# Optimization experiments

Hardware: AMD Instinct MI355X
Metric: run time of the kernel (lower is better)

## Reference

```python
import jax, jax.numpy as jnp
import numpy as np

B, N, D, D_OUT = 4, 512, 48, 48

def setup_inputs() -> dict:
    key = jax.random.key(0)
    ks = jax.random.split(key, 7)
    s1 = 1.0 / np.sqrt(2 * D)
    s2 = 1.0 / np.sqrt(2 * D)
    s3 = 1.0 / np.sqrt(D)
    return {
        "x": jax.random.normal(ks[0], (B, N, D), dtype=jnp.float32),
        "W1": jax.random.uniform(ks[1], (2 * D, 2 * D), jnp.float32, -s1, s1),
        "b1": jax.random.uniform(ks[2], (2 * D,), jnp.float32, -s1, s1),
        "W2": jax.random.uniform(ks[3], (2 * D, D), jnp.float32, -s2, s2),
        "b2": jax.random.uniform(ks[4], (D,), jnp.float32, -s2, s2),
        "W3": jax.random.uniform(ks[5], (D, D_OUT), jnp.float32, -s3, s3),
        "b3": jax.random.uniform(ks[6], (D_OUT,), jnp.float32, -s3, s3),
    }

def reference(x, W1, b1, W2, b2, W3, b3):
    # x: [B, N, D]
    Bn, Nn, Dn = x.shape
    xi = jnp.broadcast_to(x[:, :, None, :], (Bn, Nn, Nn, Dn))  # row i
    xj = jnp.broadcast_to(x[:, None, :, :], (Bn, Nn, Nn, Dn))  # col j
    pair = jnp.concatenate([xi, xj], axis=-1)  # [B,N,N,2D]
    h = jax.nn.gelu(pair @ W1 + b1, approximate=False)
    h = jax.nn.gelu(h @ W2 + b2, approximate=False)
    pair_out = h @ W3 + b3  # [B,N,N,d_out]
    mask = jnp.triu(jnp.ones((Nn, Nn), dtype=bool), 1)  # j > i masked
    pair_out = jnp.where(mask[None, :, :, None], 0.0, pair_out)
    w = jnp.linalg.norm(pair_out, axis=-1)  # [B,N,N]
    w = jnp.where(mask[None, :, :], -1e9, w)
    w = jax.nn.softmax(w, axis=-1)
    return jnp.einsum('bnj,bnjd->bnd', w, pair_out)
```

## Files before the change

### kernel.cpp

```cpp
#include <hip/hip_runtime.h>
#include <hip/hip_bf16.h>


constexpr int BATCH = 4;
constexpr int SEQ   = 512;
constexpr int DIM   = 48;
constexpr int DIM2  = 96;
constexpr int CH    = 64;

constexpr int AW  = 104;
constexpr int HW  = 72;

typedef short short8v __attribute__((ext_vector_type(8)));
typedef float float4v __attribute__((ext_vector_type(4)));
typedef unsigned int uint2v __attribute__((ext_vector_type(2)));
typedef unsigned int uint4v __attribute__((ext_vector_type(4)));

#define MFMA16(a, b, c) __builtin_amdgcn_mfma_f32_16x16x32_bf16(a, b, c, 0, 0, 0)

__device__ __forceinline__ float gelu_tanh(float x) {
    float u = x * x;
    float q = fmaf(0.10294537f, u, 2.3022077f);
    float e = __builtin_amdgcn_exp2f(x * q);
    float r = __builtin_amdgcn_rcpf(e + 1.0f);
    return fmaf(-x, r, x);
}
__device__ __forceinline__ short f2bf1(float v) {
    return (short)((__float_as_uint(v) + 0x8000u) >> 16);
}
__device__ __forceinline__ unsigned pack_bf16x2(float a, float b) {
    unsigned ua = __float_as_uint(a) + 0x8000u;
    unsigned ub = __float_as_uint(b) + 0x8000u;
    return __builtin_amdgcn_perm(ub, ua, 0x07060302u);
}
constexpr float LOG2E = 1.4426950408889634f;

__global__ __launch_bounds__(192) void uv_kernel(
    const float* __restrict__ x, const float* __restrict__ W1,
    const float* __restrict__ b1, float* __restrict__ U, float* __restrict__ V)
{
    __shared__ float sxT[DIM * 4];
    const int t = threadIdx.x;
    const int row0 = blockIdx.x * 4;
    if (t < DIM * 4) {
        int r = t / DIM, m = t - r * DIM;
        sxT[m * 4 + r] = x[(row0 + r) * DIM + m];
    }
    __syncthreads();
    const bool isU = (t < DIM2);
    const int  k   = isU ? t : (t - DIM2);
    const float* Wcol = W1 + (isU ? 0 : DIM * DIM2) + k;
    float binit = isU ? b1[k] : 0.0f;
    float a0 = binit, a1 = binit, a2 = binit, a3 = binit;
    #pragma unroll 8
    for (int m = 0; m < DIM; ++m) {
        float wv = Wcol[m * DIM2];
        const float4 xa = *(const float4*)&sxT[m * 4];
        a0 = fmaf(wv, xa.x, a0); a1 = fmaf(wv, xa.y, a1);
        a2 = fmaf(wv, xa.z, a2); a3 = fmaf(wv, xa.w, a3);
    }
    float* dst = isU ? U : V;
    dst[(row0 + 0) * DIM2 + k] = a0; dst[(row0 + 1) * DIM2 + k] = a1;
    dst[(row0 + 2) * DIM2 + k] = a2; dst[(row0 + 3) * DIM2 + k] = a3;
}

__global__ __launch_bounds__(256, 5) void pair_kernel(
    const float* __restrict__ U, const float* __restrict__ V,
    const float* __restrict__ W2, const float* __restrict__ b2,
    const float* __restrict__ W3, const float* __restrict__ b3,
    float* __restrict__ out)
{
    __shared__ __align__(16) char smem[32512];
    short* sA   = (short*)smem;
    short* sW2T = (short*)(smem + 13312);
    short* sH   = (short*)(smem + 23296);

    const int t   = threadIdx.x;
    const int bid = blockIdx.x;
    const int b   = bid & (BATCH - 1);
    const int i   = (SEQ - 1) - (bid >> 2);
    const int rowbase = b * SEQ + i;

    const int lane = t & 63;
    const int w    = t >> 6;
    const int col  = lane & 15;
    const int quad = lane >> 4;
    const int qo   = quad * 8;
    const int m4   = w * 16 + col;
    const int rbase = w * 16 + quad * 4;

    for (int idx = t; idx < DIM2 * DIM; idx += 256) {
        int k = idx / DIM, n = idx - k * DIM;
        sW2T[n * AW + k] = f2bf1(W2[idx]);
    }
    for (int idx = t; idx < DIM * DIM; idx += 256) {
        int k = idx / DIM, n = idx - k * DIM;
        sH[n * HW + k] = f2bf1(W3[idx]);
    }
    for (int idx = t; idx < CH * 16; idx += 256)
        sH[(idx >> 4) * HW + 48 + (idx & 15)] = 0;
    {
        uint4v z = {0u, 0u, 0u, 0u};
        for (int idx = t; idx < (CH * AW * 2) / 16; idx += 256)
            ((uint4v*)sA)[idx] = z;
    }
    const int pr = t >> 2;
    const int pq = t & 3;
    float4 uu[6];
    #pragma unroll
    for (int k = 0; k < 6; ++k) uu[k] = *(const float4*)&U[rowbase * DIM2 + (pq + 4 * k) * 4];
    __syncthreads();

    const short* w3b = sH + col * HW + qo;
    const short8v w300 = *(const short8v*)(w3b + 0);
    const short8v w301 = *(const short8v*)(w3b + 32);
    const short8v w310 = *(const short8v*)(w3b + 16*HW + 0);
    const short8v w311 = *(const short8v*)(w3b + 16*HW + 32);
    const short8v w320 = *(const short8v*)(w3b + 32*HW + 0);
    const short8v w321 = *(const short8v*)(w3b + 32*HW + 32);
    const float bb20 = b2[col], bb21 = b2[16 + col], bb22 = b2[32 + col];
    const float bb30 = b3[col], bb31 = b3[16 + col], bb32 = b3[32 + col];
    __syncthreads();

    float acc0 = 0.f, acc1 = 0.f, acc2 = 0.f;
    float m_run = -1e30f, l_run = 0.0f;

    for (int j0 = 0; j0 <= i; j0 += CH) {
        const int jmax = i - j0;
        const bool active = ((w << 4) <= jmax);

        if (active) {
            const float* Vb = V + (b * SEQ + j0 + pr) * DIM2 + pq * 4;
            #pragma unroll
            for (int kk = 0; kk < 6; ++kk) {
                const float4 vv = *(const float4*)(Vb + 16 * kk);
                float g0 = gelu_tanh(uu[kk].x + vv.x);
                float g1 = gelu_tanh(uu[kk].y + vv.y);
                float g2 = gelu_tanh(uu[kk].z + vv.z);
                float g3 = gelu_tanh(uu[kk].w + vv.w);
                uint2v o;
                o.x = pack_bf16x2(g0, g1);
                o.y = pack_bf16x2(g2, g3);
                *(uint2v*)&sA[pr * AW + (pq + 4 * kk) * 4] = o;
            }
        }
        __syncthreads();

        if (active) {
            const short* arow = &sA[m4 * AW + qo];
            short8v a0 = *(const short8v*)(arow + 0);
            short8v a1 = *(const short8v*)(arow + 32);
            short8v a2 = *(const short8v*)(arow + 64);
            const short* w2b = sW2T + col * AW + qo;
            float4v c0 = {0.f,0.f,0.f,0.f}, c1 = c0, c2 = c0;
            c0 = MFMA16(a0, *(const short8v*)(w2b + 0),          c0);
            c0 = MFMA16(a1, *(const short8v*)(w2b + 32),         c0);
            c0 = MFMA16(a2, *(const short8v*)(w2b + 64),         c0);
            c1 = MFMA16(a0, *(const short8v*)(w2b + 16*AW + 0),  c1);
            c1 = MFMA16(a1, *(const short8v*)(w2b + 16*AW + 32), c1);
            c1 = MFMA16(a2, *(const short8v*)(w2b + 16*AW + 64), c1);
            c2 = MFMA16(a0, *(const short8v*)(w2b + 32*AW + 0),  c2);
            c2 = MFMA16(a1, *(const short8v*)(w2b + 32*AW + 32), c2);
            c2 = MFMA16(a2, *(const short8v*)(w2b + 32*AW + 64), c2);
            #pragma unroll
            for (int r = 0; r < 4; ++r) {
                sH[(rbase + r) * HW +  0 + col] = f2bf1(gelu_tanh(c0[r] + bb20));
                sH[(rbase + r) * HW + 16 + col] = f2bf1(gelu_tanh(c1[r] + bb21));
                sH[(rbase + r) * HW + 32 + col] = f2bf1(gelu_tanh(c2[r] + bb22));
            }
        }
        __syncthreads();

        if (active) {
            const short* hrw = &sH[m4 * HW + qo];
            short8v a0 = *(const short8v*)(hrw + 0);
            short8v a1 = *(const short8v*)(hrw + 32);
            float4v c0 = {0.f,0.f,0.f,0.f}, c1 = c0, c2 = c0;
            c0 = MFMA16(a0, w300, c0); c0 = MFMA16(a1, w301, c0);
            c1 = MFMA16(a0, w310, c1); c1 = MFMA16(a1, w311, c1);
            c2 = MFMA16(a0, w320, c2); c2 = MFMA16(a1, w321, c2);
            float4v p0, p1, p2;
            float vr[4];
            #pragma unroll
            for (int r = 0; r < 4; ++r) {
                p0[r] = c0[r] + bb30; p1[r] = c1[r] + bb31; p2[r] = c2[r] + bb32;
                float ss = p0[r]*p0[r] + p1[r]*p1[r] + p2[r]*p2[r];
                ss += __shfl_xor(ss, 1);
                ss += __shfl_xor(ss, 2);
                ss += __shfl_xor(ss, 4);
                ss += __shfl_xor(ss, 8);
                vr[r] = (rbase + r <= jmax) ? __builtin_amdgcn_sqrtf(ss) : -1e30f;
            }
            float mloc = fmaxf(fmaxf(vr[0], vr[1]), fmaxf(vr[2], vr[3]));
            mloc = fmaxf(mloc, __shfl_xor(mloc, 16));
            mloc = fmaxf(mloc, __shfl_xor(mloc, 32));
            float newm = fmaxf(m_run, mloc);
            float sc = __builtin_amdgcn_exp2f((m_run - newm) * LOG2E);
            float e0 = __builtin_amdgcn_exp2f((vr[0] - newm) * LOG2E);
            float e1 = __builtin_amdgcn_exp2f((vr[1] - newm) * LOG2E);
            float e2 = __builtin_amdgcn_exp2f((vr[2] - newm) * LOG2E);
            float e3 = __builtin_amdgcn_exp2f((vr[3] - newm) * LOG2E);
            float s = (e0 + e1) + (e2 + e3);
            s += __shfl_xor(s, 16);
            s += __shfl_xor(s, 32);
            l_run = fmaf(l_run, sc, s);
            m_run = newm;
            acc0 *= sc; acc1 *= sc; acc2 *= sc;
            acc0 = fmaf(e0, p0[0], acc0); acc1 = fmaf(e0, p1[0], acc1); acc2 = fmaf(e0, p2[0], acc2);
            acc0 = fmaf(e1, p0[1], acc0); acc1 = fmaf(e1, p1[1], acc1); acc2 = fmaf(e1, p2[1], acc2);
            acc0 = fmaf(e2, p0[2], acc0); acc1 = fmaf(e2, p1[2], acc1); acc2 = fmaf(e2, p2[2], acc2);
            acc0 = fmaf(e3, p0[3], acc0); acc1 = fmaf(e3, p1[3], acc1); acc2 = fmaf(e3, p2[3], acc2);
        }
    }

    acc0 += __shfl_xor(acc0, 16); acc0 += __shfl_xor(acc0, 32);
    acc1 += __shfl_xor(acc1, 16); acc1 += __shfl_xor(acc1, 32);
    acc2 += __shfl_xor(acc2, 16); acc2 += __shfl_xor(acc2, 32);
    float* red = (float*)smem;
    __syncthreads();
    if (lane < 16) {
        red[w * 64 + lane]      = acc0;
        red[w * 64 + 16 + lane] = acc1;
        red[w * 64 + 32 + lane] = acc2;
    }
    if (lane == 0) { red[w * 64 + 48] = m_run; red[w * 64 + 49] = l_run; }
    __syncthreads();
    if (t < DIM) {
        float mm0 = red[48],       mm1 = red[64 + 48];
        float mm2 = red[128 + 48], mm3 = red[192 + 48];
        float M = fmaxf(fmaxf(mm0, mm1), fmaxf(mm2, mm3));
        float f0 = __builtin_amdgcn_exp2f((mm0 - M) * LOG2E);
        float f1 = __builtin_amdgcn_exp2f((mm1 - M) * LOG2E);
        float f2 = __builtin_amdgcn_exp2f((mm2 - M) * LOG2E);
        float f3 = __builtin_amdgcn_exp2f((mm3 - M) * LOG2E);
        float num = f0 * red[t] + f1 * red[64 + t] + f2 * red[128 + t] + f3 * red[192 + t];
        float den = f0 * red[49] + f1 * red[64 + 49] + f2 * red[128 + 49] + f3 * red[192 + 49];
        out[rowbase * DIM + t] = num / den;
    }
}

extern "C" void kernel_launch(void* const* d_in, const int* in_sizes, int n_in,
                              void* d_out, int out_size, void* d_ws, size_t ws_size,
                              hipStream_t stream) {
    const float* x  = (const float*)d_in[0];
    const float* W1 = (const float*)d_in[1];
    const float* b1 = (const float*)d_in[2];
    const float* W2 = (const float*)d_in[3];
    const float* b2 = (const float*)d_in[4];
    const float* W3 = (const float*)d_in[5];
    const float* b3 = (const float*)d_in[6];
    float* out = (float*)d_out;

    float* U = (float*)d_ws;
    float* V = U + BATCH * SEQ * DIM2;

    uv_kernel<<<BATCH * SEQ / 4, 192, 0, stream>>>(x, W1, b1, U, V);
    pair_kernel<<<BATCH * SEQ, 256, 0, stream>>>(U, V, W2, b2, W3, b3, out);
}
```

Baseline: 123.9 us.

## Make pair-kernel waves independent, dropping block barriers and holding W2 in registers

```diff
diff --git a/kernel.cpp b/kernel.cpp
--- a/kernel.cpp
+++ b/kernel.cpp
@@ -14,7 +14,6 @@
 typedef short short8v __attribute__((ext_vector_type(8)));
 typedef float float4v __attribute__((ext_vector_type(4)));
 typedef unsigned int uint2v __attribute__((ext_vector_type(2)));
-typedef unsigned int uint4v __attribute__((ext_vector_type(4)));
 
 #define MFMA16(a, b, c) __builtin_amdgcn_mfma_f32_16x16x32_bf16(a, b, c, 0, 0, 0)
 
@@ -64,16 +63,16 @@
     dst[(row0 + 2) * DIM2 + k] = a2; dst[(row0 + 3) * DIM2 + k] = a3;
 }
 
-__global__ __launch_bounds__(256, 5) void pair_kernel(
+__global__ __launch_bounds__(256, 4) void pair_kernel(
     const float* __restrict__ U, const float* __restrict__ V,
     const float* __restrict__ W2, const float* __restrict__ b2,
     const float* __restrict__ W3, const float* __restrict__ b3,
     float* __restrict__ out)
 {
-    __shared__ __align__(16) char smem[32512];
-    short* sA   = (short*)smem;
-    short* sW2T = (short*)(smem + 13312);
-    short* sH   = (short*)(smem + 23296);
+    __shared__ __align__(16) char smem[23296];
+    short* sA  = (short*)smem;
+    short* sH  = (short*)(smem + 13312);
+    float* sUi = (float*)(smem + 22528);
 
     const int t   = threadIdx.x;
     const int bid = blockIdx.x;
@@ -91,7 +90,7 @@
 
     for (int idx = t; idx < DIM2 * DIM; idx += 256) {
         int k = idx / DIM, n = idx - k * DIM;
-        sW2T[n * AW + k] = f2bf1(W2[idx]);
+        sA[n * AW + k] = f2bf1(W2[idx]);
     }
     for (int idx = t; idx < DIM * DIM; idx += 256) {
         int k = idx / DIM, n = idx - k * DIM;
@@ -99,18 +98,19 @@
     }
     for (int idx = t; idx < CH * 16; idx += 256)
         sH[(idx >> 4) * HW + 48 + (idx & 15)] = 0;
-    {
-        uint4v z = {0u, 0u, 0u, 0u};
-        for (int idx = t; idx < (CH * AW * 2) / 16; idx += 256)
-            ((uint4v*)sA)[idx] = z;
-    }
-    const int pr = t >> 2;
-    const int pq = t & 3;
-    float4 uu[6];
-    #pragma unroll
-    for (int k = 0; k < 6; ++k) uu[k] = *(const float4*)&U[rowbase * DIM2 + (pq + 4 * k) * 4];
-    __syncthreads();
-
+    if (t < DIM2) sUi[t] = U[rowbase * DIM2 + t];
+    __syncthreads();
+
+    const short* w2b = sA + col * AW + qo;
+    const short8v w200 = *(const short8v*)(w2b + 0);
+    const short8v w201 = *(const short8v*)(w2b + 32);
+    const short8v w202 = *(const short8v*)(w2b + 64);
+    const short8v w210 = *(const short8v*)(w2b + 16*AW + 0);
+    const short8v w211 = *(const short8v*)(w2b + 16*AW + 32);
+    const short8v w212 = *(const short8v*)(w2b + 16*AW + 64);
+    const short8v w220 = *(const short8v*)(w2b + 32*AW + 0);
+    const short8v w221 = *(const short8v*)(w2b + 32*AW + 32);
+    const short8v w222 = *(const short8v*)(w2b + 32*AW + 64);
     const short* w3b = sH + col * HW + qo;
     const short8v w300 = *(const short8v*)(w3b + 0);
     const short8v w301 = *(const short8v*)(w3b + 32);
@@ -122,46 +122,41 @@
     const float bb30 = b3[col], bb31 = b3[16 + col], bb32 = b3[32 + col];
     __syncthreads();
 
+    const int pr = t >> 2;
+    const int pq = t & 3;
+
     float acc0 = 0.f, acc1 = 0.f, acc2 = 0.f;
     float m_run = -1e30f, l_run = 0.0f;
 
-    for (int j0 = 0; j0 <= i; j0 += CH) {
+    for (int j0 = 0; j0 + (w << 4) <= i; j0 += CH) {
         const int jmax = i - j0;
-        const bool active = ((w << 4) <= jmax);
-
-        if (active) {
+
+        {
             const float* Vb = V + (b * SEQ + j0 + pr) * DIM2 + pq * 4;
             #pragma unroll
             for (int kk = 0; kk < 6; ++kk) {
                 const float4 vv = *(const float4*)(Vb + 16 * kk);
-                float g0 = gelu_tanh(uu[kk].x + vv.x);
-                float g1 = gelu_tanh(uu[kk].y + vv.y);
-                float g2 = gelu_tanh(uu[kk].z + vv.z);
-                float g3 = gelu_tanh(uu[kk].w + vv.w);
+                const float4 uu = *(const float4*)&sUi[(pq + 4 * kk) * 4];
+                float g0 = gelu_tanh(uu.x + vv.x);
+                float g1 = gelu_tanh(uu.y + vv.y);
+                float g2 = gelu_tanh(uu.z + vv.z);
+                float g3 = gelu_tanh(uu.w + vv.w);
                 uint2v o;
                 o.x = pack_bf16x2(g0, g1);
                 o.y = pack_bf16x2(g2, g3);
                 *(uint2v*)&sA[pr * AW + (pq + 4 * kk) * 4] = o;
             }
         }
-        __syncthreads();
-
-        if (active) {
+
+        {
             const short* arow = &sA[m4 * AW + qo];
             short8v a0 = *(const short8v*)(arow + 0);
             short8v a1 = *(const short8v*)(arow + 32);
             short8v a2 = *(const short8v*)(arow + 64);
-            const short* w2b = sW2T + col * AW + qo;
             float4v c0 = {0.f,0.f,0.f,0.f}, c1 = c0, c2 = c0;
-            c0 = MFMA16(a0, *(const short8v*)(w2b + 0),          c0);
-            c0 = MFMA16(a1, *(const short8v*)(w2b + 32),         c0);
-            c0 = MFMA16(a2, *(const short8v*)(w2b + 64),         c0);
-            c1 = MFMA16(a0, *(const short8v*)(w2b + 16*AW + 0),  c1);
-            c1 = MFMA16(a1, *(const short8v*)(w2b + 16*AW + 32), c1);
-            c1 = MFMA16(a2, *(const short8v*)(w2b + 16*AW + 64), c1);
-            c2 = MFMA16(a0, *(const short8v*)(w2b + 32*AW + 0),  c2);
-            c2 = MFMA16(a1, *(const short8v*)(w2b + 32*AW + 32), c2);
-            c2 = MFMA16(a2, *(const short8v*)(w2b + 32*AW + 64), c2);
+            c0 = MFMA16(a0, w200, c0); c0 = MFMA16(a1, w201, c0); c0 = MFMA16(a2, w202, c0);
+            c1 = MFMA16(a0, w210, c1); c1 = MFMA16(a1, w211, c1); c1 = MFMA16(a2, w212, c1);
+            c2 = MFMA16(a0, w220, c2); c2 = MFMA16(a1, w221, c2); c2 = MFMA16(a2, w222, c2);
             #pragma unroll
             for (int r = 0; r < 4; ++r) {
                 sH[(rbase + r) * HW +  0 + col] = f2bf1(gelu_tanh(c0[r] + bb20));
@@ -169,9 +164,8 @@
                 sH[(rbase + r) * HW + 32 + col] = f2bf1(gelu_tanh(c2[r] + bb22));
             }
         }
-        __syncthreads();
-
-        if (active) {
+
+        {
             const short* hrw = &sH[m4 * HW + qo];
             short8v a0 = *(const short8v*)(hrw + 0);
             short8v a1 = *(const short8v*)(hrw + 32);
```

Measured after the change: 107.5 us. -13.2%, faster.
